# Kernel optimization log

Measured on AMD Instinct MI355X. Metric: run time of the kernel, lower is better.

Reference implementation:

```python
import jax, jax.numpy as jnp
import numpy as np
from jax import lax

SCORE_THRESHOLD = 0.02
IOU_THRESHOLD = 0.5
NUM_CLASSES = 80
MAX_DETECTIONS = 10  # tf.image.non_max_suppression max_output_size in the source
ANCHORS = np.array([[1.08, 1.19], [3.42, 4.41], [6.63, 11.38], [9.42, 5.11], [16.62, 10.52]], dtype=np.float32)


def setup_inputs() -> dict:
    key = jax.random.key(0)
    k1, _ = jax.random.split(key)
    B, H, W = 16, 76, 76
    A = ANCHORS.shape[0]
    feats = jax.random.normal(k1, (B, H, W, A * (5 + NUM_CLASSES)), dtype=jnp.float32)
    anchors = jnp.asarray(ANCHORS)
    return {"feats": feats, "anchors": anchors}


def yolo_head(feats, anchors, num_classes):
    """Standard YOLOv2 decode (interpret_prediction)."""
    B, H, W, _ = feats.shape
    A = anchors.shape[0]
    feats = feats.reshape(B, H, W, A, 5 + num_classes)
    gy, gx = jnp.meshgrid(jnp.arange(H), jnp.arange(W), indexing="ij")
    grid = jnp.stack([gx, gy], axis=-1).astype(feats.dtype)  # [H,W,2] in (x,y) order
    conv_dims = jnp.array([W, H], dtype=feats.dtype)
    box_xy = (jax.nn.sigmoid(feats[..., 0:2]) + grid[None, :, :, None, :]) / conv_dims
    box_wh = jnp.exp(feats[..., 2:4]) * anchors[None, None, None, :, :] / conv_dims
    box_confidence = jax.nn.sigmoid(feats[..., 4:5])
    box_class_probs = jax.nn.softmax(feats[..., 5:], axis=-1)
    return box_xy, box_wh, box_confidence, box_class_probs


def _postprocess(feats, anchors):
    box_xy, box_wh, box_confidence, box_class_probs = yolo_head(feats, anchors, NUM_CLASSES)
    box_mins = box_xy - box_wh / 2.0
    box_maxes = box_xy + box_wh / 2.0
    # [y_min, x_min, y_max, x_max] as in the source (indices 1 then 0)
    boxes = jnp.concatenate([box_mins[..., 1:2], box_mins[..., 0:1], box_maxes[..., 1:2], box_maxes[..., 0:1]], axis=-1)
    box_scores = box_confidence * box_class_probs           # [B,H,W,A,C]
    box_classes = jnp.argmax(box_scores, axis=-1)           # [B,H,W,A]
    box_class_scores = jnp.max(box_scores, axis=-1)         # [B,H,W,A]

    # tf.boolean_mask flattens across all dims; emulate with fixed shapes by
    # marking below-threshold candidates as invalid (score -1).
    flat_boxes = boxes.reshape(-1, 4)                       # [N,4]
    flat_scores = box_class_scores.reshape(-1)              # [N]
    flat_classes = box_classes.reshape(-1)                  # [N]
    scores_work = jnp.where(flat_scores >= SCORE_THRESHOLD, flat_scores, -1.0)

    N = flat_boxes.shape[0]
    areas = jnp.maximum(flat_boxes[:, 2] - flat_boxes[:, 0], 0.0) * jnp.maximum(flat_boxes[:, 3] - flat_boxes[:, 1], 0.0)
    idx_range = jnp.arange(N)

    def step(sw, _):
        idx = jnp.argmax(sw)
        s = sw[idx]
        valid = s >= SCORE_THRESHOLD
        box = flat_boxes[idx]                               # [4] = y1,x1,y2,x2
        iy1 = jnp.maximum(box[0], flat_boxes[:, 0])
        ix1 = jnp.maximum(box[1], flat_boxes[:, 1])
        iy2 = jnp.minimum(box[2], flat_boxes[:, 2])
        ix2 = jnp.minimum(box[3], flat_boxes[:, 3])
        inter = jnp.maximum(iy2 - iy1, 0.0) * jnp.maximum(ix2 - ix1, 0.0)
        box_area = jnp.maximum(box[2] - box[0], 0.0) * jnp.maximum(box[3] - box[1], 0.0)
        iou = inter / (box_area + areas - inter + 1e-9)
        suppress = (iou > IOU_THRESHOLD) | (idx_range == idx)
        sw_new = jnp.where(valid & suppress, -1.0, sw)
        row = jnp.concatenate([box, s[None], flat_classes[idx].astype(jnp.float32)[None]])  # [6]
        row = jnp.where(valid, row, jnp.zeros_like(row))
        return sw_new, row

    _, rows = lax.scan(step, scores_work, None, length=MAX_DETECTIONS)
    return rows  # [MAX_DETECTIONS, 6] = [y1,x1,y2,x2,score,class]; zero rows are padding


def reference(feats, anchors):
    return _postprocess(feats, anchors)
```

## Files before the change

### kernel.cpp

```cpp
#include <hip/hip_runtime.h>
#include <stdint.h>

#define N_CAND 462080
#define NBINS  2048
#define HPAD   16
#define HIST_BLOCKS 96
#define COMPACT_BLOCKS 64
#define TARGET 256u
#define SMAX   1024
#define SCORE_THR 0.02f
#define DEC_BLOCKS 1805
#define C_CNT 0
#define C_BIN 16
#define C_HD  32
#define C_CD  48


__global__ __launch_bounds__(256) void decode_kernel(
    const float* __restrict__ feats,
    float* __restrict__ scores, unsigned char* __restrict__ cls,
    unsigned int* __restrict__ ctrl, unsigned int* __restrict__ hist)
{
    const int t = threadIdx.x;
    const int bid = blockIdx.x;
    const int xcd = bid & 7, bix = bid >> 3;
    const int swz = (xcd < 5 ? xcd * 226 : 1130 + (xcd - 5) * 225) + bix;
    const int ci = swz * 256 + t;

    if (bid == 0) {
        if (t == 0) { ctrl[C_HD] = 0u; ctrl[C_CD] = 0u; }
        for (int i = t; i < NBINS; i += 256) hist[i * HPAD] = 0u;
    }

    const float* __restrict__ fr = feats + (size_t)ci * 85;
    const float4* __restrict__ p = reinterpret_cast<const float4*>(fr + 4);
    float4 q[20];
#pragma unroll
    for (int i = 0; i < 20; ++i) q[i] = p[i];
    const float f84 = fr[84];

    float m = q[0].y; int cb = 0;
    if (q[0].z > m) { m = q[0].z; cb = 1; }
    if (q[0].w > m) { m = q[0].w; cb = 2; }
#pragma unroll
    for (int i = 1; i < 20; ++i) {
        const int b = i * 4 - 1;
        if (q[i].x > m) { m = q[i].x; cb = b; }
        if (q[i].y > m) { m = q[i].y; cb = b + 1; }
        if (q[i].z > m) { m = q[i].z; cb = b + 2; }
        if (q[i].w > m) { m = q[i].w; cb = b + 3; }
    }
    if (f84 > m) { m = f84; cb = 79; }

    float s0 = __expf(q[0].y - m);
    float s1 = __expf(q[0].z - m);
    float s2 = __expf(q[0].w - m);
    float s3 = 0.f;
#pragma unroll
    for (int i = 1; i < 20; ++i) {
        s0 += __expf(q[i].x - m);
        s1 += __expf(q[i].y - m);
        s2 += __expf(q[i].z - m);
        s3 += __expf(q[i].w - m);
    }
    s3 += __expf(f84 - m);
    const float ssum = (s0 + s1) + (s2 + s3);

    const float conf = 1.0f / (1.0f + __expf(-q[0].x));
    const float score = conf / ssum;
    scores[ci] = (score >= SCORE_THR) ? score : -1.0f;
    cls[ci] = (unsigned char)cb;
}

__global__ __launch_bounds__(1024) void hist_cutoff_kernel(
    const float* __restrict__ scores, unsigned int* __restrict__ hist,
    unsigned int* __restrict__ ctrl)
{
    __shared__ unsigned int lh[NBINS];
    __shared__ unsigned int pa[1024], pb[1024];
    __shared__ int lastf;
    const int t = threadIdx.x;

    lh[2 * t] = 0u; lh[2 * t + 1] = 0u;
    __syncthreads();

    for (int i = blockIdx.x * 1024 + t; i < N_CAND; i += HIST_BLOCKS * 1024) {
        float s = scores[i];
        if (s >= SCORE_THR) {
            int bin = (int)(s * (float)NBINS);
            bin = bin > (NBINS - 1) ? (NBINS - 1) : bin;
            atomicAdd(&lh[bin], 1u);
        }
    }
    __syncthreads();
    unsigned v0 = lh[2 * t], v1 = lh[2 * t + 1];
    if (v0) atomicAdd(&hist[(2 * t) * HPAD], v0);
    if (v1) atomicAdd(&hist[(2 * t + 1) * HPAD], v1);
    __syncthreads();

    if (t == 0) {
        __threadfence();
        unsigned old = atomicAdd(&ctrl[C_HD], 1u);
        lastf = (old == HIST_BLOCKS - 1) ? 1 : 0;
    }
    __syncthreads();
    if (!lastf) return;
    if (t == 0) __threadfence();
    __syncthreads();

    unsigned b0 = hist[(2 * t) * HPAD];
    unsigned b1 = hist[(2 * t + 1) * HPAD];
    lh[2 * t] = b0; lh[2 * t + 1] = b1;
    pa[t] = b0 + b1;
    __syncthreads();

    unsigned int* srcb = pa; unsigned int* dstb = pb;
    for (int off = 1; off < 1024; off <<= 1) {
        unsigned v = srcb[t] + ((t + off < 1024) ? srcb[t + off] : 0u);
        dstb[t] = v;
        __syncthreads();
        unsigned int* tmp = srcb; srcb = dstb; dstb = tmp;
    }
    unsigned St = srcb[t];
    unsigned Sn = (t < 1023) ? srcb[t + 1] : 0u;

    if (t == 0) {
        ctrl[C_CNT] = 0u;
        if (St < TARGET) ctrl[C_BIN] = 0u;
    }
    if (St >= TARGET && Sn < TARGET) {
        unsigned run = Sn + lh[2 * t + 1];
        ctrl[C_BIN] = (run >= TARGET) ? (unsigned)(2 * t + 1) : (unsigned)(2 * t);
    }
}

__device__ inline float4 decode_box(const float* __restrict__ feats,
                                    const float* __restrict__ anchors, int ci)
{
    int a = ci % 5;
    int cell = ci / 5;
    int gx = cell % 76;
    int gy = (cell / 76) % 76;
    const float* f = feats + (long long)ci * 85;
    float bx = (1.0f / (1.0f + __expf(-f[0])) + (float)gx) / 76.0f;
    float by = (1.0f / (1.0f + __expf(-f[1])) + (float)gy) / 76.0f;
    float bw = __expf(f[2]) * anchors[2 * a]     / 76.0f;
    float bh = __expf(f[3]) * anchors[2 * a + 1] / 76.0f;
    return make_float4(by - bh * 0.5f, bx - bw * 0.5f,
                       by + bh * 0.5f, bx + bw * 0.5f);
}

__global__ __launch_bounds__(1024) void compact_nms_kernel(
    const float* __restrict__ scores, unsigned int* __restrict__ ctrl,
    float* __restrict__ lscore, int* __restrict__ lidx,
    const float* __restrict__ feats, const float* __restrict__ anchors,
    const unsigned char* __restrict__ cls, float* __restrict__ out)
{
    __shared__ unsigned long long wkey[16];
    __shared__ unsigned long long bkey;
    __shared__ float4 bbox;
    __shared__ int lastf;
    const int t = threadIdx.x;

    const int cut = (int)ctrl[C_BIN];
    for (int i = blockIdx.x * 1024 + t; i < N_CAND; i += COMPACT_BLOCKS * 1024) {
        float sw = scores[i];
        if (sw >= SCORE_THR) {
            int bin = (int)(sw * (float)NBINS);
            bin = bin > (NBINS - 1) ? (NBINS - 1) : bin;
            if (bin >= cut) {
                unsigned pos = atomicAdd(&ctrl[C_CNT], 1u);
                if (pos < SMAX) { lscore[pos] = sw; lidx[pos] = i; }
            }
        }
    }
    __syncthreads();
    if (t == 0) {
        __threadfence();
        unsigned old = atomicAdd(&ctrl[C_CD], 1u);
        lastf = (old == COMPACT_BLOCKS - 1) ? 1 : 0;
    }
    __syncthreads();
    if (!lastf) return;
    if (t == 0) __threadfence();
    __syncthreads();

    unsigned cnt = ctrl[C_CNT];
    int n = (cnt < (unsigned)SMAX) ? (int)cnt : SMAX;

    unsigned long long key = 0ull;
    float4 mb = make_float4(0.f, 0.f, 0.f, 0.f);
    float  msc = 0.f, mcls = 0.f;
    unsigned midx = 0xFFFFFFFFu;
    bool aliveb = false;
    if (t < n) {
        msc  = lscore[t];
        midx = (unsigned)lidx[t];
        key  = ((unsigned long long)__float_as_uint(msc) << 32)
             | (unsigned long long)(0xFFFFFFFFu - midx);
        mb   = decode_box(feats, anchors, (int)midx);
        mcls = (float)cls[midx];
        aliveb = true;
    }

    for (int r = 0; r < 10; ++r) {
        unsigned long long k0 = aliveb ? key : 0ull;
#pragma unroll
        for (int msk = 32; msk > 0; msk >>= 1) {
            unsigned long long o = __shfl_xor(k0, msk);
            k0 = (o > k0) ? o : k0;
        }
        if ((t & 63) == 0) wkey[t >> 6] = k0;
        __syncthreads();
        if (t < 16) {
            unsigned long long v = wkey[t];
#pragma unroll
            for (int msk = 8; msk > 0; msk >>= 1) {
                unsigned long long o = __shfl_xor(v, msk);
                v = (o > v) ? o : v;
            }
            if (t == 0) bkey = v;
        }
        __syncthreads();

        unsigned long long wk = bkey;
        bool have = (wk != 0ull);
        unsigned widx = have ? (0xFFFFFFFFu - (unsigned)(wk & 0xFFFFFFFFull)) : 0xFFFFFFFFu;

        if (have && aliveb && midx == widx) {
            bbox = mb;
            out[r * 6 + 0] = mb.x;
            out[r * 6 + 1] = mb.y;
            out[r * 6 + 2] = mb.z;
            out[r * 6 + 3] = mb.w;
            out[r * 6 + 4] = msc;
            out[r * 6 + 5] = mcls;
            aliveb = false;
        }
        if (!have && t == 0) {
#pragma unroll
            for (int q = 0; q < 6; ++q) out[r * 6 + q] = 0.f;
        }
        __syncthreads();

        if (have && aliveb) {
            float4 ab = bbox;
            float aarea = fmaxf(ab.z - ab.x, 0.f) * fmaxf(ab.w - ab.y, 0.f);
            float iy1 = fmaxf(ab.x, mb.x);
            float ix1 = fmaxf(ab.y, mb.y);
            float iy2 = fminf(ab.z, mb.z);
            float ix2 = fminf(ab.w, mb.w);
            float inter = fmaxf(iy2 - iy1, 0.f) * fmaxf(ix2 - ix1, 0.f);
            float carea = fmaxf(mb.z - mb.x, 0.f) * fmaxf(mb.w - mb.y, 0.f);
            float iou = inter / (aarea + carea - inter + 1e-9f);
            if (iou > 0.5f) aliveb = false;
        }
    }
}

extern "C" void kernel_launch(void* const* d_in, const int* in_sizes, int n_in,
                              void* d_out, int out_size, void* d_ws, size_t ws_size,
                              hipStream_t stream) {
    const float* feats   = (const float*)d_in[0];
    const float* anchors = (const float*)d_in[1];
    char* ws = (char*)d_ws;

    unsigned int*   ctrl   = (unsigned int*)(ws + 0);
    unsigned int*   hist   = (unsigned int*)(ws + 256);
    float*          lscore = (float*)(ws + 131328);
    int*            lidx   = (int*)(ws + 135424);
    float*          scores = (float*)(ws + 139520);
    unsigned char*  cls    = (unsigned char*)(ws + 1987840);
    float*          out    = (float*)d_out;

    decode_kernel      <<<DEC_BLOCKS, 256, 0, stream>>>(feats, scores, cls, ctrl, hist);
    hist_cutoff_kernel <<<HIST_BLOCKS, 1024, 0, stream>>>(scores, hist, ctrl);
    compact_nms_kernel <<<COMPACT_BLOCKS, 1024, 0, stream>>>(scores, ctrl, lscore, lidx,
                                                             feats, anchors, cls, out);
}
```

Measured before the change: 57.42 us.

## Fuse histogram-cutoff and compact-NMS kernels with a device-wide flag barrier

Merges the histogram/cutoff kernel and the compaction+NMS kernel into one persistent-style kernel of 96 blocks. A spin-wait on a global flag, set by the last block after it computes the cutoff bin, replaces the kernel boundary. This removes one kernel launch and its inter-kernel gap. It relies on all 96 blocks of 1024 threads being co-resident, or the spin can deadlock. The compaction phase now also runs with 96 blocks instead of 64.

Result: slower. 60.18 us (+4.8%).

```diff
diff --git a/kernel.cpp b/kernel.cpp
--- a/kernel.cpp
+++ b/kernel.cpp
@@ -4,8 +4,7 @@
 #define N_CAND 462080
 #define NBINS  2048
 #define HPAD   16
-#define HIST_BLOCKS 96
-#define COMPACT_BLOCKS 64
+#define TBLOCKS 96
 #define TARGET 256u
 #define SMAX   1024
 #define SCORE_THR 0.02f
@@ -14,6 +13,7 @@
 #define C_BIN 16
 #define C_HD  32
 #define C_CD  48
+#define C_FLG 64
 
 
 __global__ __launch_bounds__(256) void decode_kernel(
@@ -28,7 +28,7 @@
     const int ci = swz * 256 + t;
 
     if (bid == 0) {
-        if (t == 0) { ctrl[C_HD] = 0u; ctrl[C_CD] = 0u; }
+        if (t == 0) { ctrl[C_HD] = 0u; ctrl[C_CD] = 0u; ctrl[C_FLG] = 0u; }
         for (int i = t; i < NBINS; i += 256) hist[i * HPAD] = 0u;
     }
 
@@ -70,68 +70,6 @@
     const float score = conf / ssum;
     scores[ci] = (score >= SCORE_THR) ? score : -1.0f;
     cls[ci] = (unsigned char)cb;
-}
-
-__global__ __launch_bounds__(1024) void hist_cutoff_kernel(
-    const float* __restrict__ scores, unsigned int* __restrict__ hist,
-    unsigned int* __restrict__ ctrl)
-{
-    __shared__ unsigned int lh[NBINS];
-    __shared__ unsigned int pa[1024], pb[1024];
-    __shared__ int lastf;
-    const int t = threadIdx.x;
-
-    lh[2 * t] = 0u; lh[2 * t + 1] = 0u;
-    __syncthreads();
-
-    for (int i = blockIdx.x * 1024 + t; i < N_CAND; i += HIST_BLOCKS * 1024) {
-        float s = scores[i];
-        if (s >= SCORE_THR) {
-            int bin = (int)(s * (float)NBINS);
-            bin = bin > (NBINS - 1) ? (NBINS - 1) : bin;
-            atomicAdd(&lh[bin], 1u);
-        }
-    }
-    __syncthreads();
-    unsigned v0 = lh[2 * t], v1 = lh[2 * t + 1];
-    if (v0) atomicAdd(&hist[(2 * t) * HPAD], v0);
-    if (v1) atomicAdd(&hist[(2 * t + 1) * HPAD], v1);
-    __syncthreads();
-
-    if (t == 0) {
-        __threadfence();
-        unsigned old = atomicAdd(&ctrl[C_HD], 1u);
-        lastf = (old == HIST_BLOCKS - 1) ? 1 : 0;
-    }
-    __syncthreads();
-    if (!lastf) return;
-    if (t == 0) __threadfence();
-    __syncthreads();
-
-    unsigned b0 = hist[(2 * t) * HPAD];
-    unsigned b1 = hist[(2 * t + 1) * HPAD];
-    lh[2 * t] = b0; lh[2 * t + 1] = b1;
-    pa[t] = b0 + b1;
-    __syncthreads();
-
-    unsigned int* srcb = pa; unsigned int* dstb = pb;
-    for (int off = 1; off < 1024; off <<= 1) {
-        unsigned v = srcb[t] + ((t + off < 1024) ? srcb[t + off] : 0u);
-        dstb[t] = v;
-        __syncthreads();
-        unsigned int* tmp = srcb; srcb = dstb; dstb = tmp;
-    }
-    unsigned St = srcb[t];
-    unsigned Sn = (t < 1023) ? srcb[t + 1] : 0u;
-
-    if (t == 0) {
-        ctrl[C_CNT] = 0u;
-        if (St < TARGET) ctrl[C_BIN] = 0u;
-    }
-    if (St >= TARGET && Sn < TARGET) {
-        unsigned run = Sn + lh[2 * t + 1];
-        ctrl[C_BIN] = (run >= TARGET) ? (unsigned)(2 * t + 1) : (unsigned)(2 * t);
-    }
 }
 
 __device__ inline float4 decode_box(const float* __restrict__ feats,
@@ -150,20 +88,83 @@
                        by + bh * 0.5f, bx + bw * 0.5f);
 }
 
-__global__ __launch_bounds__(1024) void compact_nms_kernel(
-    const float* __restrict__ scores, unsigned int* __restrict__ ctrl,
+__global__ __launch_bounds__(1024) void tail_kernel(
+    const float* __restrict__ scores, unsigned int* __restrict__ hist,
+    unsigned int* __restrict__ ctrl,
     float* __restrict__ lscore, int* __restrict__ lidx,
     const float* __restrict__ feats, const float* __restrict__ anchors,
     const unsigned char* __restrict__ cls, float* __restrict__ out)
 {
+    __shared__ unsigned int lh[NBINS];
+    __shared__ unsigned int pa[1024], pb[1024];
     __shared__ unsigned long long wkey[16];
     __shared__ unsigned long long bkey;
     __shared__ float4 bbox;
     __shared__ int lastf;
     const int t = threadIdx.x;
 
+    lh[2 * t] = 0u; lh[2 * t + 1] = 0u;
+    __syncthreads();
+    for (int i = blockIdx.x * 1024 + t; i < N_CAND; i += TBLOCKS * 1024) {
+        float s = scores[i];
+        if (s >= SCORE_THR) {
+            int bin = (int)(s * (float)NBINS);
+            bin = bin > (NBINS - 1) ? (NBINS - 1) : bin;
+            atomicAdd(&lh[bin], 1u);
+        }
+    }
+    __syncthreads();
+    unsigned v0 = lh[2 * t], v1 = lh[2 * t + 1];
+    if (v0) atomicAdd(&hist[(2 * t) * HPAD], v0);
+    if (v1) atomicAdd(&hist[(2 * t + 1) * HPAD], v1);
+    __syncthreads();
+
+    if (t == 0) {
+        __threadfence();
+        unsigned old = atomicAdd(&ctrl[C_HD], 1u);
+        lastf = (old == TBLOCKS - 1) ? 1 : 0;
+    }
+    __syncthreads();
+    if (lastf) {
+        if (t == 0) __threadfence();
+        __syncthreads();
+        unsigned b0 = hist[(2 * t) * HPAD];
+        unsigned b1 = hist[(2 * t + 1) * HPAD];
+        lh[2 * t] = b0; lh[2 * t + 1] = b1;
+        pa[t] = b0 + b1;
+        __syncthreads();
+        unsigned int* srcb = pa; unsigned int* dstb = pb;
+        for (int off = 1; off < 1024; off <<= 1) {
+            unsigned v = srcb[t] + ((t + off < 1024) ? srcb[t + off] : 0u);
+            dstb[t] = v;
+            __syncthreads();
+            unsigned int* tmp = srcb; srcb = dstb; dstb = tmp;
+        }
+        unsigned St = srcb[t];
+        unsigned Sn = (t < 1023) ? srcb[t + 1] : 0u;
+        if (t == 0) {
+            ctrl[C_CNT] = 0u;
+            if (St < TARGET) ctrl[C_BIN] = 0u;
+        }
+        if (St >= TARGET && Sn < TARGET) {
+            unsigned run = Sn + lh[2 * t + 1];
+            ctrl[C_BIN] = (run >= TARGET) ? (unsigned)(2 * t + 1) : (unsigned)(2 * t);
+        }
+        __syncthreads();
+        if (t == 0) {
+            __threadfence();
+            atomicExch(&ctrl[C_FLG], 1u);
+        }
+    }
+
+    if (t == 0) {
+        while (atomicAdd(&ctrl[C_FLG], 0u) == 0u) __builtin_amdgcn_s_sleep(8);
+        __threadfence();
+    }
+    __syncthreads();
+
     const int cut = (int)ctrl[C_BIN];
-    for (int i = blockIdx.x * 1024 + t; i < N_CAND; i += COMPACT_BLOCKS * 1024) {
+    for (int i = blockIdx.x * 1024 + t; i < N_CAND; i += TBLOCKS * 1024) {
         float sw = scores[i];
         if (sw >= SCORE_THR) {
             int bin = (int)(sw * (float)NBINS);
@@ -175,10 +176,11 @@
         }
     }
     __syncthreads();
+
     if (t == 0) {
         __threadfence();
         unsigned old = atomicAdd(&ctrl[C_CD], 1u);
-        lastf = (old == COMPACT_BLOCKS - 1) ? 1 : 0;
+        lastf = (old == TBLOCKS - 1) ? 1 : 0;
     }
     __syncthreads();
     if (!lastf) return;
@@ -239,7 +241,7 @@
         }
         if (!have && t == 0) {
 #pragma unroll
-            for (int q = 0; q < 6; ++q) out[r * 6 + q] = 0.f;
+            for (int qq = 0; qq < 6; ++qq) out[r * 6 + qq] = 0.f;
         }
         __syncthreads();
 
@@ -266,15 +268,14 @@
     char* ws = (char*)d_ws;
 
     unsigned int*   ctrl   = (unsigned int*)(ws + 0);
-    unsigned int*   hist   = (unsigned int*)(ws + 256);
-    float*          lscore = (float*)(ws + 131328);
-    int*            lidx   = (int*)(ws + 135424);
-    float*          scores = (float*)(ws + 139520);
-    unsigned char*  cls    = (unsigned char*)(ws + 1987840);
+    unsigned int*   hist   = (unsigned int*)(ws + 512);
+    float*          lscore = (float*)(ws + 131584);
+    int*            lidx   = (int*)(ws + 135680);
+    float*          scores = (float*)(ws + 139776);
+    unsigned char*  cls    = (unsigned char*)(ws + 1988096);
     float*          out    = (float*)d_out;
 
-    decode_kernel      <<<DEC_BLOCKS, 256, 0, stream>>>(feats, scores, cls, ctrl, hist);
-    hist_cutoff_kernel <<<HIST_BLOCKS, 1024, 0, stream>>>(scores, hist, ctrl);
-    compact_nms_kernel <<<COMPACT_BLOCKS, 1024, 0, stream>>>(scores, ctrl, lscore, lidx,
-                                                             feats, anchors, cls, out);
-}
+    decode_kernel <<<DEC_BLOCKS, 256, 0, stream>>>(feats, scores, cls, ctrl, hist);
+    tail_kernel   <<<TBLOCKS, 1024, 0, stream>>>(scores, hist, ctrl, lscore, lidx,
+                                                 feats, anchors, cls, out);
+}
```
